# Optimization experiments

Hardware: AMD Instinct MI355X
Metric: run time of the kernel (lower is better)

Reference implementation:

```python
import jax, jax.numpy as jnp
import numpy as np

NH, N = 48, 384
CARD, SUB, REPR, ENC = 16, 64, 1024, 1024
POOL_FEAT = 256 * 49


def _head_params(keys, app_size):
    k1, k2, k3 = keys
    W1 = jax.random.normal(k1, (CARD, app_size, SUB), jnp.float32) / np.sqrt(app_size)
    b1 = jnp.zeros((CARD, SUB), jnp.float32)
    W2 = jax.random.normal(k2, (CARD, REPR, SUB), jnp.float32) / np.sqrt(REPR)
    b2 = jnp.zeros((CARD, SUB), jnp.float32)
    W3 = jax.random.normal(k3, (CARD, SUB, REPR), jnp.float32) / np.sqrt(SUB)
    b3 = jnp.zeros((CARD, REPR), jnp.float32)
    return W1, b1, W2, b2, W3, b3


def setup_inputs() -> dict:
    key = jax.random.key(0)
    ks = list(jax.random.split(key, 24))
    d = {}
    d['box_features'] = jax.random.normal(ks[0], (N, POOL_FEAT), jnp.float32)
    d['feat3'] = jax.random.normal(ks[1], (1, 256, 25, 25), jnp.float32)
    d['spatial36'] = jax.random.uniform(ks[2], (NH * N, 36), jnp.float32)
    d['Wbh1'] = jax.random.normal(ks[3], (POOL_FEAT, ENC), jnp.float32) / np.sqrt(POOL_FEAT)
    d['bbh1'] = jnp.zeros(ENC, jnp.float32)
    d['Wbh2'] = jax.random.normal(ks[4], (ENC, ENC), jnp.float32) / np.sqrt(ENC)
    d['bbh2'] = jnp.zeros(ENC, jnp.float32)
    d['Wsp1'] = jax.random.normal(ks[5], (36, 128), jnp.float32) / 6.0
    d['bsp1'] = jnp.zeros(128, jnp.float32)
    d['Wsp2'] = jax.random.normal(ks[6], (128, 256), jnp.float32) / np.sqrt(128)
    d['bsp2'] = jnp.zeros(256, jnp.float32)
    d['Wsp3'] = jax.random.normal(ks[7], (256, REPR), jnp.float32) / 16.0
    d['bsp3'] = jnp.zeros(REPR, jnp.float32)
    d['Wadj'] = jax.random.normal(ks[8], (REPR, 1), jnp.float32) / 32.0
    d['badj'] = jnp.zeros(1, jnp.float32)
    for pre, app, k0 in (('A', 2 * ENC, 9), ('O', ENC, 12), ('S', ENC, 15), ('G', 256, 18)):
        W1, b1, W2, b2, W3, b3 = _head_params(ks[k0:k0 + 3], app)
        d[pre + '1W'], d[pre + '1b'] = W1, b1
        d[pre + '2W'], d[pre + '2b'] = W2, b2
        d[pre + '3W'], d[pre + '3b'] = W3, b3
    d['gln_h'] = jnp.ones(ENC, jnp.float32)
    d['bln_h'] = jnp.zeros(ENC, jnp.float32)
    d['gln_o'] = jnp.ones(ENC, jnp.float32)
    d['bln_o'] = jnp.zeros(ENC, jnp.float32)
    d['n_h'] = NH
    return d


def _attn_head(app, sp, W1, b1, W2, b2, W3, b3):
    # app [P_or_1, A], sp [P, REPR] -> relu(sum_c fc3_c(relu(fc1_c(app)*fc2_c(sp))))
    u = jnp.einsum('pa,cas->cps', app, W1) + b1[:, None, :]
    v = jnp.einsum('ps,csd->cpd', sp, W2) + b2[:, None, :]
    t = jax.nn.relu(u * v)  # broadcasts when app has leading 1
    return jax.nn.relu(jnp.einsum('cpd,cdr->pr', t, W3) + b3.sum(0))


def _msg_obj(app, sp, W1, b1, W2, b2, W3, b3):
    # app [n, ENC], sp [h, n, REPR] -> [h, n, REPR]  (object->subject messages)
    u = jnp.einsum('ne,ces->cns', app, W1) + b1[:, None, :]
    v = jnp.einsum('hns,csd->chnd', sp, W2) + b2[:, None, None, :]
    t = jax.nn.relu(u[:, None, :, :] * v)
    return jnp.einsum('chnd,cdr->hnr', t, W3) + b3.sum(0)


def _msg_hum(app, sp, W1, b1, W2, b2, W3, b3):
    # app [h, ENC], sp [h, n, REPR] -> [n, h, REPR]  (subject->object messages)
    u = jnp.einsum('he,ces->chs', app, W1) + b1[:, None, :]
    v = jnp.einsum('hns,csd->cnhd', sp, W2) + b2[:, None, None, :]
    t = jax.nn.relu(u[:, None, :, :] * v)
    return jnp.einsum('cnhd,cdr->nhr', t, W3) + b3.sum(0)


def _ln(x, g, b):
    mu = x.mean(-1, keepdims=True)
    var = jnp.mean((x - mu) ** 2, -1, keepdims=True)
    return (x - mu) * jax.lax.rsqrt(var + 1e-5) * g + b


def reference(box_features, feat3, spatial36, Wbh1, bbh1, Wbh2, bbh2,
              Wsp1, bsp1, Wsp2, bsp2, Wsp3, bsp3, Wadj, badj,
              A1W, A1b, A2W, A2b, A3W, A3b,
              O1W, O1b, O2W, O2b, O3W, O3b,
              S1W, S1b, S2W, S2b, S3W, S3b,
              G1W, G1b, G2W, G2b, G3W, G3b,
              gln_h, bln_h, gln_o, bln_o, n_h):
    h = int(n_h)
    n = box_features.shape[0]
    gfeat = feat3.mean(axis=(2, 3))  # [1, 256] (AdaptiveAvgPool2d(1) + flatten)
    # box_head MLP
    node = jax.nn.relu(box_features @ Wbh1 + bbh1)
    node = jax.nn.relu(node @ Wbh2 + bbh2)  # [n, ENC]
    # spatial_head MLP
    sp = jax.nn.relu(spatial36 @ Wsp1 + bsp1)
    sp = jax.nn.relu(sp @ Wsp2 + bsp2)
    sp = jax.nn.relu(sp @ Wsp3 + bsp3)  # [h*n, REPR]
    sp_r = sp.reshape(h, n, -1)
    x = np.repeat(np.arange(h), n)  # static pair indices
    y = np.tile(np.arange(n), h)
    h_node = node[:h]
    # one message-passing iteration (num_iter=1)
    pair_app = jnp.concatenate([h_node[x], node[y]], axis=1)  # [h*n, 2*ENC]
    w = _attn_head(pair_app, sp, A1W, A1b, A2W, A2b, A3W, A3b)
    adj = (w @ Wadj + badj).reshape(h, n)
    m_h = jax.nn.relu(jnp.sum(jax.nn.softmax(adj, axis=1)[..., None]
                              * _msg_obj(node, sp_r, O1W, O1b, O2W, O2b, O3W, O3b), axis=1))
    h_node = _ln(h_node + m_h, gln_h, bln_h)
    m_o = jax.nn.relu(jnp.sum(jax.nn.softmax(adj.T, axis=1)[..., None]
                              * _msg_hum(h_node, sp_r, S1W, S1b, S2W, S2b, S3W, S3b), axis=1))
    node = _ln(node + m_o, gln_o, bln_o)
    # static keep mask: drop pairs with identical indices (x != y)
    keep = x != y
    xk, yk = x[keep], y[keep]
    sp_k = sp_r[xk, yk]  # [Pk, REPR]
    f_pair = _attn_head(jnp.concatenate([h_node[xk], node[yk]], axis=1), sp_k,
                        A1W, A1b, A2W, A2b, A3W, A3b)
    f_glob = _attn_head(gfeat, sp_k, G1W, G1b, G2W, G2b, G3W, G3b)
    return jnp.concatenate([f_pair, f_glob], axis=1)  # [Pk, 2*REPR]
```

## Files before the change

### kernel.cpp

```cpp
#include <hip/hip_runtime.h>
#include <math.h>

#define NHH 48
#define NNN 384
#define NP  18432
#define NEC 1024

#define BM 128
#define BN 128
#define BK 32
#define KPAD 40

typedef __attribute__((ext_vector_type(8))) short short8v;
typedef __attribute__((ext_vector_type(4))) float f32x4;

__device__ __forceinline__ unsigned short f2bf(float x) {
  unsigned int u = __float_as_uint(x);
  u += 0x7fffu + ((u >> 16) & 1u);
  return (unsigned short)(u >> 16);
}
__device__ __forceinline__ float bf2f(unsigned short b) {
  return __uint_as_float(((unsigned)b) << 16);
}

__global__ __launch_bounds__(256) void convw_k(const float* __restrict__ in,
    unsigned short* __restrict__ out, int K, int N, int blocked)
{
  __shared__ float t[64][65];
  int kb = blockIdx.x * 64, nb = blockIdx.y * 64;
  const float* src; size_t stride;
  if (blocked) { src = in + (size_t)(nb >> 6) * K * 64; stride = 64; }
  else         { src = in + nb; stride = N; }
  for (int i = threadIdx.x; i < 64 * 64; i += 256) {
    int k = i >> 6, d = i & 63;
    t[d][k] = src[(size_t)(kb + k) * stride + d];
  }
  __syncthreads();
  for (int i = threadIdx.x; i < 64 * 64; i += 256) {
    int d = i >> 6, k = i & 63;
    out[(size_t)(nb + d) * K + kb + k] = f2bf(t[d][k]);
  }
}

template<int MODE, int CBF16>
__global__ __launch_bounds__(512, 4) void gemm_big(
    const unsigned short* __restrict__ A, const unsigned short* __restrict__ B,
    void* __restrict__ Cv, int M, int N, int K,
    const float* __restrict__ bias, int do_relu,
    const float* __restrict__ x1, const float* __restrict__ x2,
    float* __restrict__ part, int colofs, int swz)
{
  __shared__ unsigned short As[BM * KPAD];
  __shared__ unsigned short Bs[BN * KPAD];
  __shared__ float red4[BM][4];

  const int tid  = threadIdx.x;
  const int lane = tid & 63;
  const int wave = tid >> 6;
  const int wr = wave >> 2;
  const int wc = wave & 3;
  const int lm = lane & 15;
  const int kg = lane >> 4;

  int bx = blockIdx.x, by = blockIdx.y;
  if (swz) {
    int L = by * 8 + bx;
    int r = L & 7, q = L >> 3;
    bx = q / 18;
    by = r + 8 * (q - bx * 18);
  }
  const int m0 = by * BM, n0 = bx * BN;

  f32x4 acc[4][2];
#pragma unroll
  for (int i = 0; i < 4; ++i)
#pragma unroll
    for (int j = 0; j < 2; ++j)
      acc[i][j] = (f32x4){0.f, 0.f, 0.f, 0.f};

  const int sr = tid >> 2;
  const int sc = (tid & 3) * 8;
  const unsigned short* aptr = A + (size_t)(m0 + sr) * K + sc;
  const unsigned short* bptr = B + (size_t)(n0 + sr) * K + sc;
  const int ldsOff = sr * KPAD + sc;

  uint4 a0, b0, a1, b1;
  a0 = *(const uint4*)(aptr);
  b0 = *(const uint4*)(bptr);
  if (BK < K) { a1 = *(const uint4*)(aptr + BK); b1 = *(const uint4*)(bptr + BK); }

  auto compute = [&]() {
    const int lk = kg * 8;
    short8v af[4], bfr[2];
#pragma unroll
    for (int mi = 0; mi < 4; ++mi)
      af[mi] = *(const short8v*)&As[(wr * 64 + mi * 16 + lm) * KPAD + lk];
#pragma unroll
    for (int nj = 0; nj < 2; ++nj)
      bfr[nj] = *(const short8v*)&Bs[(wc * 32 + nj * 16 + lm) * KPAD + lk];
#pragma unroll
    for (int mi = 0; mi < 4; ++mi)
#pragma unroll
      for (int nj = 0; nj < 2; ++nj)
        acc[mi][nj] = __builtin_amdgcn_mfma_f32_16x16x32_bf16(af[mi], bfr[nj], acc[mi][nj], 0, 0, 0);
  };

  for (int k0 = 0; k0 < K; k0 += 2 * BK) {
    *(uint4*)&As[ldsOff] = a0;
    *(uint4*)&Bs[ldsOff] = b0;
    if (k0 + 2 * BK < K) { a0 = *(const uint4*)(aptr + k0 + 2 * BK); b0 = *(const uint4*)(bptr + k0 + 2 * BK); }
    __syncthreads();
    compute();
    __syncthreads();
    *(uint4*)&As[ldsOff] = a1;
    *(uint4*)&Bs[ldsOff] = b1;
    if (k0 + 3 * BK < K) { a1 = *(const uint4*)(aptr + k0 + 3 * BK); b1 = *(const uint4*)(bptr + k0 + 3 * BK); }
    __syncthreads();
    compute();
    __syncthreads();
  }

  const int rbase = m0 + wr * 64;
  const int cbase = n0 + wc * 32;

  if constexpr (MODE == 0 || MODE == 3 || MODE == 4) {
#pragma unroll
    for (int mi = 0; mi < 4; ++mi)
#pragma unroll
      for (int r = 0; r < 4; ++r) {
        int grow = rbase + mi * 16 + kg * 4 + r;
        int h = 0, n = 0;
        if constexpr (MODE == 4) { h = grow / NNN; n = grow - h * NNN; }
#pragma unroll
        for (int nj = 0; nj < 2; ++nj) {
          int gcol = cbase + nj * 16 + lm;
          float t = acc[mi][nj][r] + (bias ? bias[gcol] : 0.f);
          float v;
          if constexpr (MODE == 3)      v = fmaxf(x1[gcol] * t, 0.f);
          else if constexpr (MODE == 4) v = fmaxf((x1[(size_t)h * NEC + gcol] + x2[(size_t)n * NEC + gcol]) * t, 0.f);
          else                          v = do_relu ? fmaxf(t, 0.f) : t;
          size_t idx = (size_t)grow * N + gcol;
          if constexpr (CBF16) ((unsigned short*)Cv)[idx] = f2bf(v);
          else                 ((float*)Cv)[idx] = v;
        }
      }
  } else if constexpr (MODE == 2) {
#pragma unroll
    for (int mi = 0; mi < 4; ++mi)
#pragma unroll
      for (int r = 0; r < 4; ++r) {
        int grow = rbase + mi * 16 + kg * 4 + r;
        int h = grow / NNN, n = grow - h * NNN;
        if (n == h) continue;
        long long orow = grow - h - (n > h ? 1 : 0);
#pragma unroll
        for (int nj = 0; nj < 2; ++nj) {
          int gcol = cbase + nj * 16 + lm;
          float v = fmaxf(acc[mi][nj][r] + bias[gcol], 0.f);
          ((float*)Cv)[orow * 2048 + colofs + gcol] = v;
        }
      }
  } else if constexpr (MODE == 1) {
#pragma unroll
    for (int mi = 0; mi < 4; ++mi)
#pragma unroll
      for (int r = 0; r < 4; ++r) {
        float s = 0.f;
#pragma unroll
        for (int nj = 0; nj < 2; ++nj) {
          int gcol = cbase + nj * 16 + lm;
          float v = fmaxf(acc[mi][nj][r] + bias[gcol], 0.f);
          s = fmaf(v, x1[gcol], s);
        }
#pragma unroll
        for (int off2 = 1; off2 < 16; off2 <<= 1) s += __shfl_xor(s, off2);
        if (lm == 0) red4[wr * 64 + mi * 16 + kg * 4 + r][wc] = s;
      }
    __syncthreads();
    if (tid < BM) {
      part[(size_t)(m0 + tid) * 8 + bx] = red4[tid][0] + red4[tid][1] + red4[tid][2] + red4[tid][3];
    }
  }
}

template<int MODE, int ABF16, int BBF16, int CBF16>
__global__ __launch_bounds__(256) void gemm_mfma(
    const void* __restrict__ Av, const void* __restrict__ Bv, long long ldbBlock,
    void* __restrict__ Cv, int M, int N, int K, int Ks,
    const float* __restrict__ bias, int do_relu,
    const float* __restrict__ x1, const float* __restrict__ x2,
    float* __restrict__ part, int colofs, int swz)
{
  __shared__ unsigned short As[BM * KPAD];
  __shared__ unsigned short Bs[BN * KPAD];

  const float* Af = (const float*)Av;
  const unsigned short* Ab = (const unsigned short*)Av;
  const float* Bf = (const float*)Bv;
  const unsigned short* Bb = (const unsigned short*)Bv;

  const int tid  = threadIdx.x;
  const int lane = tid & 63;
  const int wave = tid >> 6;
  const int wr = wave >> 1, wc = wave & 1;
  const int lm = lane & 15;
  const int kg = lane >> 4;

  int bx = blockIdx.x, by = blockIdx.y, bz = blockIdx.z;
  if (swz == 2) {
    int gy = gridDim.y;
    int ntile = gy * gridDim.z;
    int L = (bz * gy + by) * 8 + bx;
    int r = L & 7, q = L >> 3;
    int tpx = ntile >> 3;
    int tile = r * tpx + (q >> 3);
    bx = q & 7;
    bz = tile / gy;
    by = tile - bz * gy;
  }
  const int m0 = by * BM, n0 = bx * BN;
  const int kbeg = bz * Ks;
  const int kend = min(K, kbeg + Ks);

  f32x4 acc[4][4];
#pragma unroll
  for (int i = 0; i < 4; ++i)
#pragma unroll
    for (int j = 0; j < 4; ++j)
      acc[i][j] = (f32x4){0.f, 0.f, 0.f, 0.f};

  const int bn = tid & 127;
  const int kb = (tid >> 7) * 16;
  const float* bsrc = nullptr; long long bstride = 0;
  if constexpr (!BBF16) {
    int gcol = n0 + bn;
    if (ldbBlock) { bsrc = Bf + (long long)(gcol >> 6) * ldbBlock + (gcol & 63); bstride = 64; }
    else          { bsrc = Bf + gcol; bstride = N; }
  }

  uint4 pa0 = {0,0,0,0}, pa1 = {0,0,0,0};
  uint2 qa0 = {0,0}, qa1 = {0,0}, qa2 = {0,0}, qa3 = {0,0};
  uint4 pb0 = {0,0,0,0}, pb1 = {0,0,0,0};

  auto fetchA = [&](int k0) {
    if constexpr (ABF16) {
      int m = tid >> 1, kh = (tid & 1) * 16;
      int gm = m0 + m;
      pa0 = (uint4){0,0,0,0}; pa1 = (uint4){0,0,0,0};
      if (gm < M) {
        const uint4* s = (const uint4*)(Ab + (size_t)gm * K + k0 + kh);
        pa0 = s[0]; pa1 = s[1];
      }
    } else {
#define LOADA_F32(J, DST) { \
      int m = (tid >> 3) + J * 32; int k = (tid & 7) * 4; \
      int gm = m0 + m, gk = k0 + k; \
      float x0=0.f, x1v=0.f, x2v=0.f, x3=0.f; \
      if (gm < M) { const float* src = Af + (long long)gm * K + gk; \
        if (gk + 3 < K) { float4 v = *(const float4*)src; x0=v.x; x1v=v.y; x2v=v.z; x3=v.w; } \
        else { if (gk < K) x0 = src[0]; if (gk+1 < K) x1v = src[1]; \
               if (gk+2 < K) x2v = src[2]; if (gk+3 < K) x3 = src[3]; } } \
      DST.x = (unsigned)f2bf(x0)  | ((unsigned)f2bf(x1v) << 16); \
      DST.y = (unsigned)f2bf(x2v) | ((unsigned)f2bf(x3)  << 16); }
      LOADA_F32(0, qa0) LOADA_F32(1, qa1) LOADA_F32(2, qa2) LOADA_F32(3, qa3)
#undef LOADA_F32
    }
  };
  auto fetchB = [&](int k0) {
    if constexpr (BBF16) {
      int nrow = tid >> 1, kh = (tid & 1) * 16;
      const uint4* s = (const uint4*)(Bb + (size_t)(n0 + nrow) * K + k0 + kh);
      pb0 = s[0]; pb1 = s[1];
    } else {
#define PACKB(I, DST) { int g0 = k0 + kb + 2*I, g1 = g0 + 1; \
      float a = (g0 < K) ? bsrc[(long long)g0 * bstride] : 0.f; \
      float c = (g1 < K) ? bsrc[(long long)g1 * bstride] : 0.f; \
      DST = (unsigned)f2bf(a) | ((unsigned)f2bf(c) << 16); }
      PACKB(0, pb0.x) PACKB(1, pb0.y) PACKB(2, pb0.z) PACKB(3, pb0.w)
      PACKB(4, pb1.x) PACKB(5, pb1.y) PACKB(6, pb1.z) PACKB(7, pb1.w)
#undef PACKB
    }
  };
  auto stage = [&]() {
    if constexpr (ABF16) {
      int m = tid >> 1, kh = (tid & 1) * 16;
      *(uint4*)&As[m * KPAD + kh]     = pa0;
      *(uint4*)&As[m * KPAD + kh + 8] = pa1;
    } else {
      int m = tid >> 3, k = (tid & 7) * 4;
      *(uint2*)&As[(m      ) * KPAD + k] = qa0;
      *(uint2*)&As[(m +  32) * KPAD + k] = qa1;
      *(uint2*)&As[(m +  64) * KPAD + k] = qa2;
      *(uint2*)&As[(m +  96) * KPAD + k] = qa3;
    }
    if constexpr (BBF16) {
      int nrow = tid >> 1, kh = (tid & 1) * 16;
      *(uint4*)&Bs[nrow * KPAD + kh]     = pb0;
      *(uint4*)&Bs[nrow * KPAD + kh + 8] = pb1;
    } else {
      *(uint4*)&Bs[bn * KPAD + kb]     = pb0;
      *(uint4*)&Bs[bn * KPAD + kb + 8] = pb1;
    }
  };

  fetchA(kbeg); fetchB(kbeg);
  for (int k0 = kbeg; k0 < kend; k0 += BK) {
    stage();
    int kn = k0 + BK;
    if (kn < kend) { fetchA(kn); fetchB(kn); }
    __syncthreads();
    {
      const int lk = kg * 8;
      short8v af[4], bfr[4];
#pragma unroll
      for (int mi = 0; mi < 4; ++mi)
        af[mi] = *(const short8v*)&As[(wr * 64 + mi * 16 + lm) * KPAD + lk];
#pragma unroll
      for (int nj = 0; nj < 4; ++nj)
        bfr[nj] = *(const short8v*)&Bs[(wc * 64 + nj * 16 + lm) * KPAD + lk];
#pragma unroll
      for (int mi = 0; mi < 4; ++mi)
#pragma unroll
        for (int nj = 0; nj < 4; ++nj)
          acc[mi][nj] = __builtin_amdgcn_mfma_f32_16x16x32_bf16(af[mi], bfr[nj], acc[mi][nj], 0, 0, 0);
    }
    __syncthreads();
  }

  const int rbase = m0 + wr * 64;
  const int cbase = n0 + wc * 64;

  if constexpr (MODE == 0) {
#pragma unroll
    for (int mi = 0; mi < 4; ++mi)
#pragma unroll
      for (int r = 0; r < 4; ++r) {
        int grow = rbase + mi * 16 + kg * 4 + r;
        if (grow >= M) continue;
#pragma unroll
        for (int nj = 0; nj < 4; ++nj) {
          int gcol = cbase + nj * 16 + lm;
          float t = acc[mi][nj][r] + (bias ? bias[gcol] : 0.f);
          float v = do_relu ? fmaxf(t, 0.f) : t;
          size_t idx = (size_t)grow * N + gcol;
          if constexpr (CBF16) ((unsigned short*)Cv)[idx] = f2bf(v);
          else                 ((float*)Cv)[idx] = v;
        }
      }
  } else if constexpr (MODE == 5) {
    size_t zofs = (size_t)bz * M;
#pragma unroll
    for (int mi = 0; mi < 4; ++mi)
#pragma unroll
      for (int r = 0; r < 4; ++r) {
        int grow = rbase + mi * 16 + kg * 4 + r;
        if (grow >= M) continue;
#pragma unroll
        for (int nj = 0; nj < 4; ++nj) {
          int gcol = cbase + nj * 16 + lm;
          part[(zofs + grow) * N + gcol] = acc[mi][nj][r];
        }
      }
  }
}

__global__ __launch_bounds__(256) void ksum_k(const float* __restrict__ P,
    const float* __restrict__ bias, int do_relu, float* __restrict__ C,
    int MN, int N, int S)
{
  int i = blockIdx.x * 256 + threadIdx.x;
  if (i < MN) {
    float s = 0.f;
    for (int z = 0; z < S; ++z) s += P[(size_t)z * MN + i];
    if (bias) s += bias[i % N];
    C[i] = do_relu ? fmaxf(s, 0.f) : s;
  }
}

__global__ __launch_bounds__(256) void tw_k(const unsigned short* __restrict__ V,
    const float* __restrict__ uO, const float* __restrict__ soft, float* __restrict__ tw)
{
  int h = blockIdx.x;
  int j = blockIdx.y * 256 + threadIdx.x;
  const float* srow = soft + h * NNN;
  float s = 0.f;
  for (int n = 0; n < NNN; ++n) {
    float v = bf2f(V[((size_t)h * NNN + n) * NEC + j]);
    float t = fmaxf(uO[(size_t)n * NEC + j] * v, 0.f);
    s = fmaf(srow[n], t, s);
  }
  tw[(size_t)h * NEC + j] = s;
}

__global__ __launch_bounds__(256) void two_k(const unsigned short* __restrict__ V,
    const float* __restrict__ uS, const float* __restrict__ softT, float* __restrict__ two)
{
  int n = blockIdx.x;
  int j = blockIdx.y * 256 + threadIdx.x;
  const float* srow = softT + n * NHH;
  float s = 0.f;
#pragma unroll 8
  for (int h = 0; h < NHH; ++h) {
    float v = bf2f(V[((size_t)h * NNN + n) * NEC + j]);
    float t = fmaxf(uS[(size_t)h * NEC + j] * v, 0.f);
    s = fmaf(srow[h], t, s);
  }
  two[(size_t)n * NEC + j] = s;
}

__global__ void adjfin_k(const float* __restrict__ part, const float* __restrict__ badj,
                         float* __restrict__ adj)
{
  int p = blockIdx.x * blockDim.x + threadIdx.x;
  if (p < NP) {
    float s = badj[0];
#pragma unroll
    for (int c = 0; c < 8; ++c) s += part[(size_t)p * 8 + c];
    adj[p] = s;
  }
}

__global__ __launch_bounds__(64) void softmax_row_k(const float* __restrict__ adj,
                                                    float* __restrict__ soft)
{
  __shared__ float buf[NNN];
  int h = blockIdx.x, t = threadIdx.x;
  float mx = -1e30f;
  for (int n = t; n < NNN; n += 64) { float v = adj[h * NNN + n]; buf[n] = v; mx = fmaxf(mx, v); }
#pragma unroll
  for (int off = 32; off >= 1; off >>= 1) mx = fmaxf(mx, __shfl_xor(mx, off));
  float s = 0.f;
  for (int n = t; n < NNN; n += 64) { float e = expf(buf[n] - mx); buf[n] = e; s += e; }
#pragma unroll
  for (int off = 32; off >= 1; off >>= 1) s += __shfl_xor(s, off);
  float inv = 1.f / s;
  for (int n = t; n < NNN; n += 64) soft[h * NNN + n] = buf[n] * inv;
}

__global__ __launch_bounds__(64) void softmaxT_k(const float* __restrict__ adj,
                                                 float* __restrict__ softT)
{
  int n = blockIdx.x, t = threadIdx.x;
  float v = (t < NHH) ? adj[t * NNN + n] : -1e30f;
  float mx = v;
#pragma unroll
  for (int off = 32; off >= 1; off >>= 1) mx = fmaxf(mx, __shfl_xor(mx, off));
  float e = (t < NHH) ? expf(v - mx) : 0.f;
  float s = e;
#pragma unroll
  for (int off = 32; off >= 1; off >>= 1) s += __shfl_xor(s, off);
  if (t < NHH) softT[n * NHH + t] = e / s;
}

__global__ __launch_bounds__(256) void ln_k(const float* __restrict__ x, const float* __restrict__ m,
    const float* __restrict__ g, const float* __restrict__ b, float* __restrict__ out)
{
  int r = blockIdx.x, t = threadIdx.x;
  __shared__ float rs[4], rs2[4];
  const float* xr = x + (size_t)r * NEC;
  const float* mr = m + (size_t)r * NEC;
  float s = 0.f, s2 = 0.f;
  for (int j = t; j < NEC; j += 256) { float v = xr[j] + mr[j]; s += v; s2 = fmaf(v, v, s2); }
#pragma unroll
  for (int off = 32; off >= 1; off >>= 1) { s += __shfl_xor(s, off); s2 += __shfl_xor(s2, off); }
  if ((t & 63) == 0) { rs[t >> 6] = s; rs2[t >> 6] = s2; }
  __syncthreads();
  s = rs[0] + rs[1] + rs[2] + rs[3];
  s2 = rs2[0] + rs2[1] + rs2[2] + rs2[3];
  float mean = s * (1.f / NEC);
  float var = s2 * (1.f / NEC) - mean * mean;
  float rstd = rsqrtf(var + 1e-5f);
  float* o = out + (size_t)r * NEC;
  for (int j = t; j < NEC; j += 256) {
    float v = xr[j] + mr[j];
    o[j] = (v - mean) * rstd * g[j] + b[j];
  }
}

__global__ __launch_bounds__(64) void gfeat_k(const float* __restrict__ feat3,
                                              float* __restrict__ gfeat)
{
  int ch = blockIdx.x, t = threadIdx.x;
  float s = 0.f;
  for (int i = t; i < 625; i += 64) s += feat3[ch * 625 + i];
#pragma unroll
  for (int off = 32; off >= 1; off >>= 1) s += __shfl_xor(s, off);
  if (t == 0) gfeat[ch] = s * (1.f / 625.f);
}

__global__ __launch_bounds__(256) void b3sum_k(const float* __restrict__ b3,
                                               float* __restrict__ out)
{
  int r = blockIdx.x * 256 + threadIdx.x;
  if (r < NEC) {
    float s = 0.f;
#pragma unroll
    for (int c = 0; c < 16; ++c) s += b3[c * NEC + r];
    out[r] = s;
  }
}

extern "C" void kernel_launch(void* const* d_in, const int* in_sizes, int n_in,
                              void* d_out, int out_size, void* d_ws, size_t ws_size,
                              hipStream_t stream)
{
  const float* box   = (const float*)d_in[0];
  const float* feat3 = (const float*)d_in[1];
  const float* sp36  = (const float*)d_in[2];
  const float* Wbh1  = (const float*)d_in[3];
  const float* bbh1  = (const float*)d_in[4];
  const float* Wbh2  = (const float*)d_in[5];
  const float* bbh2  = (const float*)d_in[6];
  const float* Wsp1  = (const float*)d_in[7];
  const float* bsp1  = (const float*)d_in[8];
  const float* Wsp2  = (const float*)d_in[9];
  const float* bsp2  = (const float*)d_in[10];
  const float* Wsp3  = (const float*)d_in[11];
  const float* bsp3  = (const float*)d_in[12];
  const float* Wadj  = (const float*)d_in[13];
  const float* badj  = (const float*)d_in[14];
  const float* A1W = (const float*)d_in[15]; const float* A1b = (const float*)d_in[16];
  const float* A2W = (const float*)d_in[17]; const float* A2b = (const float*)d_in[18];
  const float* A3W = (const float*)d_in[19]; const float* A3b = (const float*)d_in[20];
  const float* O1W = (const float*)d_in[21]; const float* O1b = (const float*)d_in[22];
  const float* O2W = (const float*)d_in[23]; const float* O2b = (const float*)d_in[24];
  const float* O3W = (const float*)d_in[25]; const float* O3b = (const float*)d_in[26];
  const float* S1W = (const float*)d_in[27]; const float* S1b = (const float*)d_in[28];
  const float* S2W = (const float*)d_in[29]; const float* S2b = (const float*)d_in[30];
  const float* S3W = (const float*)d_in[31]; const float* S3b = (const float*)d_in[32];
  const float* G1W = (const float*)d_in[33]; const float* G1b = (const float*)d_in[34];
  const float* G2W = (const float*)d_in[35]; const float* G2b = (const float*)d_in[36];
  const float* G3W = (const float*)d_in[37]; const float* G3b = (const float*)d_in[38];
  const float* gln_h = (const float*)d_in[39]; const float* bln_h = (const float*)d_in[40];
  const float* gln_o = (const float*)d_in[41]; const float* bln_o = (const float*)d_in[42];
  (void)in_sizes; (void)n_in; (void)out_size; (void)ws_size;

  char* base = (char*)d_ws;
  unsigned short* Vb  = (unsigned short*)base;
  float* partial      = (float*)base;
  unsigned short* s1  = Vb;
  unsigned short* s2  = Vb + (size_t)NP * 128;
  unsigned short* SPb = (unsigned short*)(base + (size_t)NP * NEC * 2);
  float* f = (float*)(base + (size_t)NP * NEC * 4);
  size_t off = 0;
  auto alloc = [&](size_t n) { float* p = f + off; off += n; return p; };
  float* node1 = alloc(384 * NEC);
  float* node  = alloc(384 * NEC);
  float* hnode1= alloc(48 * NEC);
  float* node2 = alloc(384 * NEC);
  float* uhA   = alloc(48 * NEC);
  float* unA   = alloc(384 * NEC);
  float* uO    = alloc(384 * NEC);
  float* uS    = alloc(48 * NEC);
  float* uh2   = alloc(48 * NEC);
  float* un2   = alloc(384 * NEC);
  float* uG    = alloc(NEC);
  float* gfeat = alloc(256);
  float* b3A = alloc(NEC); float* b3O = alloc(NEC); float* b3S = alloc(NEC); float* b3G = alloc(NEC);
  float* part  = alloc((size_t)NP * 8);
  float* adj   = alloc(NP);
  float* soft  = alloc(NP);
  float* softT = alloc(NP);
  float* twb   = alloc(48 * NEC);
  float* twob  = alloc(384 * NEC);
  float* m_h   = alloc(48 * NEC);
  float* m_o   = alloc(384 * NEC);
  unsigned short* wb = (unsigned short*)(f + off);
  size_t wo = 0;
  auto walloc = [&](size_t n) { unsigned short* p = wb + wo; wo += n; return p; };
  unsigned short* A2Wb  = walloc((size_t)NEC * NEC);
  unsigned short* O2Wb  = walloc((size_t)NEC * NEC);
  unsigned short* S2Wb  = walloc((size_t)NEC * NEC);
  unsigned short* G2Wb  = walloc((size_t)NEC * NEC);
  unsigned short* A3Wb  = walloc((size_t)NEC * NEC);
  unsigned short* G3Wb  = walloc((size_t)NEC * NEC);
  unsigned short* Wsp3b = walloc((size_t)NEC * 256);
  unsigned short* Wsp2b = walloc((size_t)256 * 128);

  auto gS = [&](const float* A, const float* B, long long lb, float* C,
                int M, int N, int K, const float* bias, int relu, int S) {
    int Ks = ((K + S * BK - 1) / (S * BK)) * BK;
    dim3 grid(N / BN, (M + BM - 1) / BM, S);
    hipLaunchKernelGGL((gemm_mfma<5, 0, 0, 0>), grid, dim3(256), 0, stream,
                       A, B, lb, nullptr, M, N, K, Ks, nullptr, 0,
                       nullptr, nullptr, partial, 0, 2);
    int MN = M * N;
    hipLaunchKernelGGL(ksum_k, dim3((MN + 255) / 256), dim3(256), 0, stream,
                       partial, bias, relu, C, MN, N, S);
  };
  auto convw = [&](const float* W, unsigned short* Wb2, int K, int N, int blocked) {
    dim3 g(K / 64, N / 64);
    hipLaunchKernelGGL(convw_k, g, dim3(256), 0, stream, W, Wb2, K, N, blocked);
  };

  convw(A2W, A2Wb, NEC, NEC, 1);
  convw(O2W, O2Wb, NEC, NEC, 1);
  convw(S2W, S2Wb, NEC, NEC, 1);
  convw(G2W, G2Wb, NEC, NEC, 1);
  convw(A3W, A3Wb, NEC, NEC, 0);
  convw(G3W, G3Wb, NEC, NEC, 0);
  convw(Wsp3, Wsp3b, 256, NEC, 0);
  convw(Wsp2, Wsp2b, 128, 256, 0);

  gfeat_k<<<256, 64, 0, stream>>>(feat3, gfeat);
  b3sum_k<<<4, 256, 0, stream>>>(A3b, b3A);
  b3sum_k<<<4, 256, 0, stream>>>(O3b, b3O);
  b3sum_k<<<4, 256, 0, stream>>>(S3b, b3S);
  b3sum_k<<<4, 256, 0, stream>>>(G3b, b3G);

  gS(box,   Wbh1, 0, node1, 384, NEC, 12544, bbh1, 1, 32);
  gS(node1, Wbh2, 0, node,  384, NEC, NEC,   bbh2, 1, 16);

  dim3 gBig(8, NP / BM);

  {
    dim3 g1(1, NP / BM); dim3 g2(2, NP / BM);
    hipLaunchKernelGGL((gemm_mfma<0, 0, 0, 1>), g1, dim3(256), 0, stream,
                       sp36, Wsp1, 0LL, s1, NP, 128, 36, 36, bsp1, 1, nullptr, nullptr, nullptr, 0, 0);
    hipLaunchKernelGGL((gemm_big<0, 1>), g2, dim3(512), 0, stream,
                       s1, Wsp2b, s2, NP, 256, 128, bsp2, 1, nullptr, nullptr, nullptr, 0, 0);
    hipLaunchKernelGGL((gemm_big<0, 1>), gBig, dim3(512), 0, stream,
                       s2, Wsp3b, SPb, NP, NEC, 256, bsp3, 1, nullptr, nullptr, nullptr, 0, 1);
  }

  gS(node, A1W,             2048LL * 64, uhA, 48,  NEC, NEC, A1b,    0, 16);
  gS(node, A1W + 1024 * 64, 2048LL * 64, unA, 384, NEC, NEC, nullptr, 0, 16);
  hipLaunchKernelGGL((gemm_big<4, 1>), gBig, dim3(512), 0, stream,
                     SPb, A2Wb, Vb, NP, NEC, NEC, A2b, 0, uhA, unA, nullptr, 0, 1);
  hipLaunchKernelGGL((gemm_big<1, 0>), gBig, dim3(512), 0, stream,
                     Vb, A3Wb, nullptr, NP, NEC, NEC, b3A, 1, Wadj, nullptr, part, 0, 1);
  adjfin_k<<<(NP + 255) / 256, 256, 0, stream>>>(part, badj, adj);
  softmax_row_k<<<NHH, 64, 0, stream>>>(adj, soft);
  softmaxT_k<<<NNN, 64, 0, stream>>>(adj, softT);

  gS(node, O1W, 1024LL * 64, uO, 384, NEC, NEC, O1b, 0, 16);
  hipLaunchKernelGGL((gemm_big<0, 1>), gBig, dim3(512), 0, stream,
                     SPb, O2Wb, Vb, NP, NEC, NEC, O2b, 0, nullptr, nullptr, nullptr, 0, 1);
  tw_k<<<dim3(NHH, 4), 256, 0, stream>>>(Vb, uO, soft, twb);
  gS(twb, O3W, 0, m_h, 48, NEC, NEC, b3O, 1, 16);
  ln_k<<<NHH, 256, 0, stream>>>(node, m_h, gln_h, bln_h, hnode1);

  gS(hnode1, S1W, 1024LL * 64, uS, 48, NEC, NEC, S1b, 0, 16);
  hipLaunchKernelGGL((gemm_big<0, 1>), gBig, dim3(512), 0, stream,
                     SPb, S2Wb, Vb, NP, NEC, NEC, S2b, 0, nullptr, nullptr, nullptr, 0, 1);
  two_k<<<dim3(NNN, 4), 256, 0, stream>>>(Vb, uS, softT, twob);
  gS(twob, S3W, 0, m_o, 384, NEC, NEC, b3S, 1, 16);
  ln_k<<<NNN, 256, 0, stream>>>(node, m_o, gln_o, bln_o, node2);

  gS(hnode1, A1W,             2048LL * 64, uh2, 48,  NEC, NEC, A1b,    0, 16);
  gS(node2,  A1W + 1024 * 64, 2048LL * 64, un2, 384, NEC, NEC, nullptr, 0, 16);
  hipLaunchKernelGGL((gemm_big<4, 1>), gBig, dim3(512), 0, stream,
                     SPb, A2Wb, Vb, NP, NEC, NEC, A2b, 0, uh2, un2, nullptr, 0, 1);
  hipLaunchKernelGGL((gemm_big<2, 0>), gBig, dim3(512), 0, stream,
                     Vb, A3Wb, (float*)d_out, NP, NEC, NEC, b3A, 1, nullptr, nullptr, nullptr, 0, 1);

  {
    dim3 g1(8, 1);
    hipLaunchKernelGGL((gemm_mfma<0, 0, 0, 0>), g1, dim3(256), 0, stream,
                       gfeat, G1W, 256LL * 64, uG, 1, NEC, 256, 256, G1b, 0, nullptr, nullptr, nullptr, 0, 0);
  }
  hipLaunchKernelGGL((gemm_big<3, 1>), gBig, dim3(512), 0, stream,
                     SPb, G2Wb, Vb, NP, NEC, NEC, G2b, 0, uG, nullptr, nullptr, 0, 1);
  hipLaunchKernelGGL((gemm_big<2, 0>), gBig, dim3(512), 0, stream,
                     Vb, G3Wb, (float*)d_out, NP, NEC, NEC, b3G, 1, nullptr, nullptr, nullptr, 1024, 1);
}
```

Baseline: 916.6 us.

## Rewrite big GEMM with direct global-to-LDS loads and 64x64 wave tiles

Replaces the 512-thread register-staged double-buffered GEMM with a 256-thread kernel that copies A/B tiles straight into LDS using global_load_lds 16-byte transfers. Each wave now computes a 64x64 output tile (4x4 MFMA accumulators) instead of 64x32, raising MFMA work per LDS fragment load. The aim is to cut VGPR staging and LDS write instructions. In exchange, LDS padding is removed, which may cause bank conflicts, and the loop no longer prefetches the next K slice while computing. Fewer waves per block also lowers latency hiding.

```diff
diff --git a/kernel.cpp b/kernel.cpp
--- a/kernel.cpp
+++ b/kernel.cpp
@@ -21,6 +21,12 @@
 }
 __device__ __forceinline__ float bf2f(unsigned short b) {
   return __uint_as_float(((unsigned)b) << 16);
+}
+
+__device__ __forceinline__ void gload16(const unsigned short* g, unsigned short* l) {
+  __builtin_amdgcn_global_load_lds(
+      (const __attribute__((address_space(1))) unsigned int*)g,
+      (__attribute__((address_space(3))) unsigned int*)l, 16, 0, 0);
 }
 
 __global__ __launch_bounds__(256) void convw_k(const float* __restrict__ in,
@@ -43,22 +49,21 @@
 }
 
 template<int MODE, int CBF16>
-__global__ __launch_bounds__(512, 4) void gemm_big(
+__global__ __launch_bounds__(256) void gemm_lds(
     const unsigned short* __restrict__ A, const unsigned short* __restrict__ B,
     void* __restrict__ Cv, int M, int N, int K,
     const float* __restrict__ bias, int do_relu,
     const float* __restrict__ x1, const float* __restrict__ x2,
     float* __restrict__ part, int colofs, int swz)
 {
-  __shared__ unsigned short As[BM * KPAD];
-  __shared__ unsigned short Bs[BN * KPAD];
-  __shared__ float red4[BM][4];
+  __shared__ unsigned short As[BM * BK];
+  __shared__ unsigned short Bs[BN * BK];
+  __shared__ float red2[BM][2];
 
   const int tid  = threadIdx.x;
   const int lane = tid & 63;
   const int wave = tid >> 6;
-  const int wr = wave >> 2;
-  const int wc = wave & 3;
+  const int wr = wave >> 1, wc = wave & 1;
   const int lm = lane & 15;
   const int kg = lane >> 4;
 
@@ -71,57 +76,50 @@
   }
   const int m0 = by * BM, n0 = bx * BN;
 
-  f32x4 acc[4][2];
+  f32x4 acc[4][4];
 #pragma unroll
   for (int i = 0; i < 4; ++i)
 #pragma unroll
-    for (int j = 0; j < 2; ++j)
+    for (int j = 0; j < 4; ++j)
       acc[i][j] = (f32x4){0.f, 0.f, 0.f, 0.f};
 
-  const int sr = tid >> 2;
-  const int sc = (tid & 3) * 8;
-  const unsigned short* aptr = A + (size_t)(m0 + sr) * K + sc;
-  const unsigned short* bptr = B + (size_t)(n0 + sr) * K + sc;
-  const int ldsOff = sr * KPAD + sc;
-
-  uint4 a0, b0, a1, b1;
-  a0 = *(const uint4*)(aptr);
-  b0 = *(const uint4*)(bptr);
-  if (BK < K) { a1 = *(const uint4*)(aptr + BK); b1 = *(const uint4*)(bptr + BK); }
-
-  auto compute = [&]() {
-    const int lk = kg * 8;
-    short8v af[4], bfr[2];
-#pragma unroll
-    for (int mi = 0; mi < 4; ++mi)
-      af[mi] = *(const short8v*)&As[(wr * 64 + mi * 16 + lm) * KPAD + lk];
-#pragma unroll
-    for (int nj = 0; nj < 2; ++nj)
-      bfr[nj] = *(const short8v*)&Bs[(wc * 32 + nj * 16 + lm) * KPAD + lk];
-#pragma unroll
-    for (int mi = 0; mi < 4; ++mi)
-#pragma unroll
-      for (int nj = 0; nj < 2; ++nj)
-        acc[mi][nj] = __builtin_amdgcn_mfma_f32_16x16x32_bf16(af[mi], bfr[nj], acc[mi][nj], 0, 0, 0);
-  };
-
-  for (int k0 = 0; k0 < K; k0 += 2 * BK) {
-    *(uint4*)&As[ldsOff] = a0;
-    *(uint4*)&Bs[ldsOff] = b0;
-    if (k0 + 2 * BK < K) { a0 = *(const uint4*)(aptr + k0 + 2 * BK); b0 = *(const uint4*)(bptr + k0 + 2 * BK); }
+  const int srow = wave * 32 + (lane >> 2);
+  const int scol = (lane & 3) * 8;
+  const unsigned short* aSrc0 = A + (size_t)(m0 + srow) * K + scol;
+  const unsigned short* aSrc1 = A + (size_t)(m0 + srow + 16) * K + scol;
+  const unsigned short* bSrc0 = B + (size_t)(n0 + srow) * K + scol;
+  const unsigned short* bSrc1 = B + (size_t)(n0 + srow + 16) * K + scol;
+  unsigned short* aDst0 = &As[(wave * 32) * BK];
+  unsigned short* aDst1 = &As[(wave * 32 + 16) * BK];
+  unsigned short* bDst0 = &Bs[(wave * 32) * BK];
+  unsigned short* bDst1 = &Bs[(wave * 32 + 16) * BK];
+
+  for (int k0 = 0; k0 < K; k0 += BK) {
+    gload16(aSrc0 + k0, aDst0);
+    gload16(aSrc1 + k0, aDst1);
+    gload16(bSrc0 + k0, bDst0);
+    gload16(bSrc1 + k0, bDst1);
     __syncthreads();
-    compute();
+    {
+      const int lk = kg * 8;
+      short8v af[4], bfr[4];
+#pragma unroll
+      for (int mi = 0; mi < 4; ++mi)
+        af[mi] = *(const short8v*)&As[(wr * 64 + mi * 16 + lm) * BK + lk];
+#pragma unroll
+      for (int nj = 0; nj < 4; ++nj)
+        bfr[nj] = *(const short8v*)&Bs[(wc * 64 + nj * 16 + lm) * BK + lk];
+#pragma unroll
+      for (int mi = 0; mi < 4; ++mi)
+#pragma unroll
+        for (int nj = 0; nj < 4; ++nj)
+          acc[mi][nj] = __builtin_amdgcn_mfma_f32_16x16x32_bf16(af[mi], bfr[nj], acc[mi][nj], 0, 0, 0);
+    }
     __syncthreads();
-    *(uint4*)&As[ldsOff] = a1;
-    *(uint4*)&Bs[ldsOff] = b1;
-    if (k0 + 3 * BK < K) { a1 = *(const uint4*)(aptr + k0 + 3 * BK); b1 = *(const uint4*)(bptr + k0 + 3 * BK); }
-    __syncthreads();
-    compute();
-    __syncthreads();
   }
 
   const int rbase = m0 + wr * 64;
-  const int cbase = n0 + wc * 32;
+  const int cbase = n0 + wc * 64;
 
   if constexpr (MODE == 0 || MODE == 3 || MODE == 4) {
 #pragma unroll
@@ -132,7 +130,7 @@
         int h = 0, n = 0;
         if constexpr (MODE == 4) { h = grow / NNN; n = grow - h * NNN; }
 #pragma unroll
-        for (int nj = 0; nj < 2; ++nj) {
+        for (int nj = 0; nj < 4; ++nj) {
           int gcol = cbase + nj * 16 + lm;
           float t = acc[mi][nj][r] + (bias ? bias[gcol] : 0.f);
           float v;
@@ -154,7 +152,7 @@
         if (n == h) continue;
         long long orow = grow - h - (n > h ? 1 : 0);
 #pragma unroll
-        for (int nj = 0; nj < 2; ++nj) {
+        for (int nj = 0; nj < 4; ++nj) {
           int gcol = cbase + nj * 16 + lm;
           float v = fmaxf(acc[mi][nj][r] + bias[gcol], 0.f);
           ((float*)Cv)[orow * 2048 + colofs + gcol] = v;
@@ -167,18 +165,18 @@
       for (int r = 0; r < 4; ++r) {
         float s = 0.f;
 #pragma unroll
-        for (int nj = 0; nj < 2; ++nj) {
+        for (int nj = 0; nj < 4; ++nj) {
           int gcol = cbase + nj * 16 + lm;
           float v = fmaxf(acc[mi][nj][r] + bias[gcol], 0.f);
           s = fmaf(v, x1[gcol], s);
         }
 #pragma unroll
         for (int off2 = 1; off2 < 16; off2 <<= 1) s += __shfl_xor(s, off2);
-        if (lm == 0) red4[wr * 64 + mi * 16 + kg * 4 + r][wc] = s;
+        if (lm == 0) red2[wr * 64 + mi * 16 + kg * 4 + r][wc] = s;
       }
     __syncthreads();
     if (tid < BM) {
-      part[(size_t)(m0 + tid) * 8 + bx] = red4[tid][0] + red4[tid][1] + red4[tid][2] + red4[tid][3];
+      part[(size_t)(m0 + tid) * 8 + bx] = red2[tid][0] + red2[tid][1];
     }
   }
 }
@@ -617,31 +615,31 @@
     dim3 g1(1, NP / BM); dim3 g2(2, NP / BM);
     hipLaunchKernelGGL((gemm_mfma<0, 0, 0, 1>), g1, dim3(256), 0, stream,
                        sp36, Wsp1, 0LL, s1, NP, 128, 36, 36, bsp1, 1, nullptr, nullptr, nullptr, 0, 0);
-    hipLaunchKernelGGL((gemm_big<0, 1>), g2, dim3(512), 0, stream,
+    hipLaunchKernelGGL((gemm_lds<0, 1>), g2, dim3(256), 0, stream,
                        s1, Wsp2b, s2, NP, 256, 128, bsp2, 1, nullptr, nullptr, nullptr, 0, 0);
-    hipLaunchKernelGGL((gemm_big<0, 1>), gBig, dim3(512), 0, stream,
+    hipLaunchKernelGGL((gemm_lds<0, 1>), gBig, dim3(256), 0, stream,
                        s2, Wsp3b, SPb, NP, NEC, 256, bsp3, 1, nullptr, nullptr, nullptr, 0, 1);
   }
 
   gS(node, A1W,             2048LL * 64, uhA, 48,  NEC, NEC, A1b,    0, 16);
   gS(node, A1W + 1024 * 64, 2048LL * 64, unA, 384, NEC, NEC, nullptr, 0, 16);
-  hipLaunchKernelGGL((gemm_big<4, 1>), gBig, dim3(512), 0, stream,
+  hipLaunchKernelGGL((gemm_lds<4, 1>), gBig, dim3(256), 0, stream,
                      SPb, A2Wb, Vb, NP, NEC, NEC, A2b, 0, uhA, unA, nullptr, 0, 1);
-  hipLaunchKernelGGL((gemm_big<1, 0>), gBig, dim3(512), 0, stream,
+  hipLaunchKernelGGL((gemm_lds<1, 0>), gBig, dim3(256), 0, stream,
                      Vb, A3Wb, nullptr, NP, NEC, NEC, b3A, 1, Wadj, nullptr, part, 0, 1);
   adjfin_k<<<(NP + 255) / 256, 256, 0, stream>>>(part, badj, adj);
   softmax_row_k<<<NHH, 64, 0, stream>>>(adj, soft);
   softmaxT_k<<<NNN, 64, 0, stream>>>(adj, softT);
 
   gS(node, O1W, 1024LL * 64, uO, 384, NEC, NEC, O1b, 0, 16);
-  hipLaunchKernelGGL((gemm_big<0, 1>), gBig, dim3(512), 0, stream,
+  hipLaunchKernelGGL((gemm_lds<0, 1>), gBig, dim3(256), 0, stream,
                      SPb, O2Wb, Vb, NP, NEC, NEC, O2b, 0, nullptr, nullptr, nullptr, 0, 1);
   tw_k<<<dim3(NHH, 4), 256, 0, stream>>>(Vb, uO, soft, twb);
   gS(twb, O3W, 0, m_h, 48, NEC, NEC, b3O, 1, 16);
   ln_k<<<NHH, 256, 0, stream>>>(node, m_h, gln_h, bln_h, hnode1);
 
   gS(hnode1, S1W, 1024LL * 64, uS, 48, NEC, NEC, S1b, 0, 16);
-  hipLaunchKernelGGL((gemm_big<0, 1>), gBig, dim3(512), 0, stream,
+  hipLaunchKernelGGL((gemm_lds<0, 1>), gBig, dim3(256), 0, stream,
                      SPb, S2Wb, Vb, NP, NEC, NEC, S2b, 0, nullptr, nullptr, nullptr, 0, 1);
   two_k<<<dim3(NNN, 4), 256, 0, stream>>>(Vb, uS, softT, twob);
   gS(twob, S3W, 0, m_o, 384, NEC, NEC, b3S, 1, 16);
@@ -649,9 +647,9 @@
 
   gS(hnode1, A1W,             2048LL * 64, uh2, 48,  NEC, NEC, A1b,    0, 16);
   gS(node2,  A1W + 1024 * 64, 2048LL * 64, un2, 384, NEC, NEC, nullptr, 0, 16);
-  hipLaunchKernelGGL((gemm_big<4, 1>), gBig, dim3(512), 0, stream,
+  hipLaunchKernelGGL((gemm_lds<4, 1>), gBig, dim3(256), 0, stream,
                      SPb, A2Wb, Vb, NP, NEC, NEC, A2b, 0, uh2, un2, nullptr, 0, 1);
-  hipLaunchKernelGGL((gemm_big<2, 0>), gBig, dim3(512), 0, stream,
+  hipLaunchKernelGGL((gemm_lds<2, 0>), gBig, dim3(256), 0, stream,
                      Vb, A3Wb, (float*)d_out, NP, NEC, NEC, b3A, 1, nullptr, nullptr, nullptr, 0, 1);
 
   {
@@ -659,8 +657,8 @@
     hipLaunchKernelGGL((gemm_mfma<0, 0, 0, 0>), g1, dim3(256), 0, stream,
                        gfeat, G1W, 256LL * 64, uG, 1, NEC, 256, 256, G1b, 0, nullptr, nullptr, nullptr, 0, 0);
   }
-  hipLaunchKernelGGL((gemm_big<3, 1>), gBig, dim3(512), 0, stream,
+  hipLaunchKernelGGL((gemm_lds<3, 1>), gBig, dim3(256), 0, stream,
                      SPb, G2Wb, Vb, NP, NEC, NEC, G2b, 0, uG, nullptr, nullptr, 0, 1);
-  hipLaunchKernelGGL((gemm_big<2, 0>), gBig, dim3(512), 0, stream,
+  hipLaunchKernelGGL((gemm_lds<2, 0>), gBig, dim3(256), 0, stream,
                      Vb, G3Wb, (float*)d_out, NP, NEC, NEC, b3G, 1, nullptr, nullptr, nullptr, 1024, 1);
 }
```

Result: slower. 1.028 ms (+12.1%).
